# Kernel optimization log

Hardware: AMD Instinct MI355X
Metric: run time of the kernel (lower is better)

## Reference

```python
import jax, jax.numpy as jnp
import numpy as np
from jax import lax

PERM_AD = np.array([3, 0, 1, 6, 4, 2, 7, 8, 5])  # angular-difference kernel permutation
IDX_HD_POS = np.array([0, 3, 6]); IDX_HD_NEG = np.array([2, 5, 8])
IDX_VD_POS = np.array([0, 1, 2]); IDX_VD_NEG = np.array([6, 7, 8])
TOP_K = 1
THETA = 1.0


def conv2d_3x3(x, w, b):
    # x: [B,C,H,W], w: [O,I,3,3], b: [O]; stride 1, padding 1
    out = lax.conv_general_dilated(x, w, window_strides=(1, 1), padding=((1, 1), (1, 1)),
                                   dimension_numbers=('NCHW', 'OIHW', 'NCHW'))
    return out + b[None, :, None, None]


def setup_inputs() -> dict:
    key = jax.random.key(0)
    ks = jax.random.split(key, 12)
    B, C, H, W, E = 16, 64, 128, 128, 5

    def winit(k, shape, fan_in):
        return jax.random.normal(k, shape, jnp.float32) * (1.0 / np.sqrt(fan_in))

    return {
        'x': jax.random.normal(ks[0], (B, C, H, W), jnp.float32),
        'noise': jax.random.normal(ks[1], (B, E), jnp.float32),
        'w_gate': winit(ks[2], (C, E), C), 'b_gate': jnp.zeros((E,), jnp.float32),
        'w_noise': winit(ks[3], (C, E), C), 'b_noise': jnp.zeros((E,), jnp.float32),
        'w1': winit(ks[4], (C, C, 3, 3), C * 9), 'b1': jnp.zeros((C,), jnp.float32),
        'w_cd': winit(ks[5], (C, C, 3, 3), C * 9), 'b_cd': jnp.zeros((C,), jnp.float32),
        'w_hd': winit(ks[6], (C, C, 3), C * 3), 'b_hd': jnp.zeros((C,), jnp.float32),
        'w_vd': winit(ks[7], (C, C, 3), C * 3), 'b_vd': jnp.zeros((C,), jnp.float32),
        'w_ad': winit(ks[8], (C, C, 3, 3), C * 9), 'b_ad': jnp.zeros((C,), jnp.float32),
    }


def reference(x, noise, w_gate, b_gate, w_noise, b_noise,
              w1, b1, w_cd, b_cd, w_hd, b_hd, w_vd, b_vd, w_ad, b_ad):
    B, C, H, W = x.shape
    E = w_gate.shape[1]

    # ---- NoisyTopkRouter on globally pooled features ----
    pooled = x.mean(axis=(2, 3))                      # [B, C]
    logits = pooled @ w_gate + b_gate                 # [B, E]
    noise_logits = pooled @ w_noise + b_noise         # [B, E]
    noisy = logits + noise * jax.nn.softplus(noise_logits)
    topv, topi = lax.top_k(noisy, TOP_K)              # [B, k]
    sparse = jnp.full_like(noisy, -jnp.inf)
    sparse = sparse.at[jnp.arange(B)[:, None], topi].set(topv)
    gates = jax.nn.softmax(sparse, axis=-1)           # [B, E]; 0 for unselected, gate weight otherwise

    # ---- Difference-convolution expert kernels ----
    wcd_f = w_cd.reshape(C, C, 9)
    wcd = wcd_f.at[:, :, 4].add(-wcd_f.sum(-1)).reshape(C, C, 3, 3)   # center = w4 - sum(all)
    whd = jnp.zeros((C, C, 9), x.dtype).at[:, :, IDX_HD_POS].set(w_hd).at[:, :, IDX_HD_NEG].set(-w_hd).reshape(C, C, 3, 3)
    wvd = jnp.zeros((C, C, 9), x.dtype).at[:, :, IDX_VD_POS].set(w_vd).at[:, :, IDX_VD_NEG].set(-w_vd).reshape(C, C, 3, 3)
    wad_f = w_ad.reshape(C, C, 9)
    wad = (wad_f - THETA * wad_f[:, :, PERM_AD]).reshape(C, C, 3, 3)

    outs = jnp.stack([
        conv2d_3x3(x, w1, b1),
        conv2d_3x3(x, wcd, b_cd),
        conv2d_3x3(x, whd, b_hd),
        conv2d_3x3(x, wvd, b_vd),
        conv2d_3x3(x, wad, b_ad),
    ], axis=0)                                        # [E, B, C, H, W]

    # ---- SparseDispatcher.combine: per-example softmax over flattened depth, gate-weighted scatter-add ----
    flat = outs.reshape(E, B, C * H * W)
    sm = jax.nn.softmax(flat, axis=-1)                # softmax over depth dim, as in combine()
    combined = jnp.einsum('ebd,be->bd', sm, gates)    # gates are 0 for non-dispatched (expert,example) pairs
    return combined.reshape(B, C, H, W)
```

## Files before the change

kernel.cpp:

```cpp
#include <hip/hip_runtime.h>
#include <math.h>

#define B_  16
#define C_  64
#define HW_ 128
#define E_  5

typedef __bf16  bf16x8 __attribute__((ext_vector_type(8)));
typedef float   f32x4  __attribute__((ext_vector_type(4)));

#define WS_WEFFB   0
#define WS_BIAS    368640
#define WS_POOL    369920
#define WS_Z       374016
#define WS_EIDX    374080
#define WS_XT      374144
#define WS_EXP     33928576
#define WS_NEED_A  67483008ull
#define WS_NEED_B  33928576ull

static __device__ __forceinline__ unsigned short f2bf(float f) {
    unsigned int u = __float_as_uint(f);
    unsigned int r = (u + 0x7fffu + ((u >> 16) & 1u)) >> 16;
    return (unsigned short)r;
}

__global__ __launch_bounds__(256) void transpose_pool_kernel(
        const float* __restrict__ x, unsigned short* __restrict__ x_t,
        float* __restrict__ pooled) {
    int bid = blockIdx.x;
    int b = bid >> 7, row = bid & 127;
    int t = threadIdx.x;
    int wave = t >> 6, l = t & 63;
    int half = l >> 5;
    int c4 = l & 31;

    __shared__ unsigned short T[128][72];

    const float* xb = x + (size_t)b * (64 * 16384) + row * 128;

    #pragma unroll
    for (int it = 0; it < 8; it++) {
        int ci = wave * 16 + it * 2 + half;
        float4 v = *(const float4*)(xb + (size_t)ci * 16384 + c4 * 4);
        float p = v.x + v.y + v.z + v.w;
        p += __shfl_down(p, 16, 32);
        p += __shfl_down(p, 8, 32);
        p += __shfl_down(p, 4, 32);
        p += __shfl_down(p, 2, 32);
        p += __shfl_down(p, 1, 32);
        if (c4 == 0) atomicAdd(&pooled[b * 64 + ci], p * (1.0f / 16384.0f));
        int colb = c4 * 4;
        T[colb + 0][ci] = f2bf(v.x);
        T[colb + 1][ci] = f2bf(v.y);
        T[colb + 2][ci] = f2bf(v.z);
        T[colb + 3][ci] = f2bf(v.w);
    }
    __syncthreads();

    unsigned short* dst = x_t + ((size_t)(b * 128 + row) * 128) * 64;
    #pragma unroll
    for (int k = 0; k < 4; k++) {
        int chunk = t + k * 256;
        int col = chunk >> 3, c8 = chunk & 7;
        uint4 vv = *(const uint4*)&T[col][c8 * 8];
        *(uint4*)(dst + col * 64 + c8 * 8) = vv;
    }
}

__global__ void route_kernel(const float* __restrict__ pooled,
                             const float* __restrict__ noise,
                             const float* __restrict__ w_gate, const float* __restrict__ b_gate,
                             const float* __restrict__ w_noise, const float* __restrict__ b_noise,
                             int* __restrict__ expert_idx) {
    int b = threadIdx.x;
    if (b >= B_) return;
    float best = -1e30f;
    int bi = 0;
    for (int e = 0; e < E_; e++) {
        float lg = b_gate[e], nz = b_noise[e];
        for (int c = 0; c < C_; c++) {
            float pv = pooled[b * C_ + c];
            lg += pv * w_gate[c * E_ + e];
            nz += pv * w_noise[c * E_ + e];
        }
        float sp = log1pf(expf(nz));
        float v = lg + noise[b * E_ + e] * sp;
        if (v > best) { best = v; bi = e; }
    }
    expert_idx[b] = bi;
}

__global__ void build_w_kernel(const float* __restrict__ w1, const float* __restrict__ w_cd,
                               const float* __restrict__ w_hd, const float* __restrict__ w_vd,
                               const float* __restrict__ w_ad,
                               const float* __restrict__ b1, const float* __restrict__ b_cd,
                               const float* __restrict__ b_hd, const float* __restrict__ b_vd,
                               const float* __restrict__ b_ad,
                               unsigned short* __restrict__ wEffB, float* __restrict__ biasEff) {
    int gid = blockIdx.x * 256 + threadIdx.x;
    if (gid < E_ * 36864) {
        int e   = gid / 36864;
        int r   = gid % 36864;
        int g   = r / 18432;
        int r2  = r % 18432;
        int tap = r2 / 2048;
        int r3  = r2 % 2048;
        int q   = r3 / 512;
        int r4  = r3 % 512;
        int co  = r4 / 8;
        int j   = r4 % 8;
        int ci = g * 32 + q * 8 + j;
        int base9 = (co * 64 + ci) * 9;
        int base3 = (co * 64 + ci) * 3;
        float v = 0.f;
        if (e == 0) {
            v = w1[base9 + tap];
        } else if (e == 1) {
            if (tap == 4) {
                float s = 0.f;
                #pragma unroll
                for (int k = 0; k < 9; k++) s += w_cd[base9 + k];
                v = w_cd[base9 + 4] - s;
            } else {
                v = w_cd[base9 + tap];
            }
        } else if (e == 2) {
            int m = tap % 3;
            if (m == 0) v = w_hd[base3 + tap / 3];
            else if (m == 2) v = -w_hd[base3 + tap / 3];
        } else if (e == 3) {
            if (tap < 3) v = w_vd[base3 + tap];
            else if (tap >= 6) v = -w_vd[base3 + tap - 6];
        } else {
            const int PERM[9] = {3, 0, 1, 6, 4, 2, 7, 8, 5};
            v = w_ad[base9 + tap] - w_ad[base9 + PERM[tap]];
        }
        wEffB[gid] = f2bf(v);
    } else if (gid < E_ * 36864 + E_ * 64) {
        int jj = gid - E_ * 36864;
        int e = jj / 64, co = jj % 64;
        const float* bs;
        switch (e) {
            case 0: bs = b1; break;
            case 1: bs = b_cd; break;
            case 2: bs = b_hd; break;
            case 3: bs = b_vd; break;
            default: bs = b_ad; break;
        }
        biasEff[jj] = bs[co];
    }
}

__global__ __launch_bounds__(256) void conv_mfma_kernel(
        const unsigned short* __restrict__ x_t, const unsigned short* __restrict__ wEffB,
        const float* __restrict__ biasEff, const int* __restrict__ expert_idx,
        unsigned short* __restrict__ expw, float* __restrict__ outf,
        float* __restrict__ Z, int direct_f32) {
    int bid = blockIdx.x;
    int b = bid >> 6;
    int rem = bid & 63;
    int rg = rem >> 1;
    int ch = rem & 1;

    int t = threadIdx.x;
    int wave = t >> 6;
    int lane = t & 63;
    int ln = lane & 15;
    int q = lane >> 4;

    int e = expert_idx[b];

    __shared__ __align__(16) unsigned short A_lds[9 * 4 * 66 * 8];
    __shared__ __align__(16) unsigned short Xs[6 * 4 * 68 * 8];
    __shared__ float zs[4];

    f32x4 acc[4][4];
    #pragma unroll
    for (int i = 0; i < 4; i++)
        #pragma unroll
        for (int jn = 0; jn < 4; jn++)
            acc[i][jn] = (f32x4){0.f, 0.f, 0.f, 0.f};

    const unsigned short* xb = x_t + (size_t)b * (128 * 128 * 64);
    const unsigned short* we = wEffB + (size_t)e * 36864;

    for (int g = 0; g < 2; g++) {
        const uint4* asrc = (const uint4*)(we + g * 18432);
        for (int j = t; j < 2304; j += 256) {
            int slotrow = j >> 6;
            int m = j & 63;
            *(uint4*)&A_lds[(slotrow * 66 + m) * 8] = asrc[j];
        }
        for (int j = t; j < 1584; j += 256) {
            int xr = j / 264;
            int r2 = j % 264;
            int col = r2 >> 2;
            int qq = r2 & 3;
            int irow = rg * 4 - 1 + xr;
            int icol = ch * 64 - 1 + col;
            uint4 v = make_uint4(0, 0, 0, 0);
            if ((unsigned)irow < 128u && (unsigned)icol < 128u)
                v = *(const uint4*)(xb + ((size_t)irow * 128 + icol) * 64 + g * 32 + qq * 8);
            *(uint4*)&Xs[((xr * 4 + qq) * 68 + col) * 8] = v;
        }
        __syncthreads();

        #pragma unroll
        for (int tap = 0; tap < 9; tap++) {
            int dr = tap / 3, dc = tap % 3;
            bf16x8 af[4], bfr[4];
            #pragma unroll
            for (int mt = 0; mt < 4; mt++)
                af[mt] = *(const bf16x8*)&A_lds[((tap * 4 + q) * 66 + mt * 16 + ln) * 8];
            int xr = wave + dr;
            #pragma unroll
            for (int t4 = 0; t4 < 4; t4++)
                bfr[t4] = *(const bf16x8*)&Xs[((xr * 4 + q) * 68 + t4 * 16 + ln + dc) * 8];
            #pragma unroll
            for (int mt = 0; mt < 4; mt++)
                #pragma unroll
                for (int t4 = 0; t4 < 4; t4++)
                    acc[mt][t4] = __builtin_amdgcn_mfma_f32_16x16x32_bf16(
                        af[mt], bfr[t4], acc[mt][t4], 0, 0, 0);
        }
        __syncthreads();
    }

    int orow = rg * 4 + wave;
    float bsum = 0.f;
    size_t obase = (size_t)b * (64 * 16384);
    #pragma unroll
    for (int mt = 0; mt < 4; mt++) {
        float4 bias4 = *(const float4*)(biasEff + e * 64 + mt * 16 + q * 4);
        const float* bp = (const float*)&bias4;
        #pragma unroll
        for (int r = 0; r < 4; r++) {
            int co = mt * 16 + q * 4 + r;
            size_t cb = obase + (size_t)co * 16384 + (size_t)orow * 128;
            #pragma unroll
            for (int t4 = 0; t4 < 4; t4++) {
                float ev = __expf(acc[mt][t4][r] + bp[r]);
                bsum += ev;
                int ocol = ch * 64 + t4 * 16 + ln;
                if (direct_f32) outf[cb + ocol] = ev;
                else            expw[cb + ocol] = f2bf(ev);
            }
        }
    }
    for (int off = 32; off; off >>= 1) bsum += __shfl_down(bsum, off, 64);
    if (lane == 0) zs[wave] = bsum;
    __syncthreads();
    if (t == 0) atomicAdd(&Z[b], zs[0] + zs[1] + zs[2] + zs[3]);
}

__global__ __launch_bounds__(256) void scale_bf16_kernel(
        const unsigned short* __restrict__ expw, const float* __restrict__ Z,
        float* __restrict__ out) {
    int gid = blockIdx.x * 256 + threadIdx.x;
    int b = gid >> 17;
    __shared__ float sinv;
    if (threadIdx.x == 0) sinv = 1.0f / Z[b];
    __syncthreads();
    uint4 r = ((const uint4*)expw)[gid];
    float4 o0, o1;
    o0.x = __uint_as_float(r.x << 16) * sinv;
    o0.y = __uint_as_float(r.x & 0xffff0000u) * sinv;
    o0.z = __uint_as_float(r.y << 16) * sinv;
    o0.w = __uint_as_float(r.y & 0xffff0000u) * sinv;
    o1.x = __uint_as_float(r.z << 16) * sinv;
    o1.y = __uint_as_float(r.z & 0xffff0000u) * sinv;
    o1.z = __uint_as_float(r.w << 16) * sinv;
    o1.w = __uint_as_float(r.w & 0xffff0000u) * sinv;
    ((float4*)out)[gid * 2] = o0;
    ((float4*)out)[gid * 2 + 1] = o1;
}

__global__ __launch_bounds__(256) void scale_inplace_kernel(
        float* __restrict__ out, const float* __restrict__ Z) {
    int gid = blockIdx.x * 256 + threadIdx.x;
    int b = gid >> 18;
    __shared__ float sinv;
    if (threadIdx.x == 0) sinv = 1.0f / Z[b];
    __syncthreads();
    float4 v = ((float4*)out)[gid];
    v.x *= sinv; v.y *= sinv; v.z *= sinv; v.w *= sinv;
    ((float4*)out)[gid] = v;
}

extern "C" void kernel_launch(void* const* d_in, const int* in_sizes, int n_in,
                              void* d_out, int out_size, void* d_ws, size_t ws_size,
                              hipStream_t stream) {
    const float* x       = (const float*)d_in[0];
    const float* noise   = (const float*)d_in[1];
    const float* w_gate  = (const float*)d_in[2];
    const float* b_gate  = (const float*)d_in[3];
    const float* w_noise = (const float*)d_in[4];
    const float* b_noise = (const float*)d_in[5];
    const float* w1      = (const float*)d_in[6];
    const float* b1      = (const float*)d_in[7];
    const float* w_cd    = (const float*)d_in[8];
    const float* b_cd    = (const float*)d_in[9];
    const float* w_hd    = (const float*)d_in[10];
    const float* b_hd    = (const float*)d_in[11];
    const float* w_vd    = (const float*)d_in[12];
    const float* b_vd    = (const float*)d_in[13];
    const float* w_ad    = (const float*)d_in[14];
    const float* b_ad    = (const float*)d_in[15];

    char* ws = (char*)d_ws;
    unsigned short* wEffB   = (unsigned short*)(ws + WS_WEFFB);
    float*          biasEff = (float*)(ws + WS_BIAS);
    float*          pooled  = (float*)(ws + WS_POOL);
    float*          Zbuf    = (float*)(ws + WS_Z);
    int*            eidx    = (int*)(ws + WS_EIDX);
    unsigned short* x_t     = (unsigned short*)(ws + WS_XT);
    unsigned short* expw    = (unsigned short*)(ws + WS_EXP);

    float* out = (float*)d_out;
    int mode_a = (ws_size >= WS_NEED_A) ? 1 : 0;

    hipMemsetAsync(pooled, 0, 4160, stream);

    transpose_pool_kernel<<<B_ * 128, 256, 0, stream>>>(x, x_t, pooled);
    route_kernel<<<1, 64, 0, stream>>>(pooled, noise, w_gate, b_gate, w_noise, b_noise, eidx);
    build_w_kernel<<<(E_ * 36864 + E_ * 64 + 255) / 256, 256, 0, stream>>>(
        w1, w_cd, w_hd, w_vd, w_ad, b1, b_cd, b_hd, b_vd, b_ad, wEffB, biasEff);
    conv_mfma_kernel<<<1024, 256, 0, stream>>>(x_t, wEffB, biasEff, eidx,
                                               expw, out, Zbuf, mode_a ? 0 : 1);
    if (mode_a)
        scale_bf16_kernel<<<8192, 256, 0, stream>>>(expw, Zbuf, out);
    else
        scale_inplace_kernel<<<16384, 256, 0, stream>>>(out, Zbuf);
}
```

Measured before the change: 232.2 us.

## Fuse all stages into one cooperative persistent kernel with grid syncs

Replaces the chain of transpose/pool, route, weight-build, conv and rescale launches with a single cooperative kernel. Grid-wide syncs separate the phases, and the conv exps stay in registers so the final softmax scale is applied before one fp32 store, with no intermediate bf16 buffer and no separate scale pass. Weight A-fragments are now read directly from global memory instead of being staged in LDS, which lowers LDS use so that 4 blocks of 256 threads fit per CU. The cost is three grid.sync barriers and a dependence on cooperative launch, with the old multi-kernel path kept as a fallback.

```diff
diff --git a/kernel.cpp b/kernel.cpp
--- a/kernel.cpp
+++ b/kernel.cpp
@@ -1,9 +1,11 @@
 #include <hip/hip_runtime.h>
+#include <hip/hip_cooperative_groups.h>
 #include <math.h>
+
+namespace cg = cooperative_groups;
 
 #define B_  16
 #define C_  64
-#define HW_ 128
 #define E_  5
 
 typedef __bf16  bf16x8 __attribute__((ext_vector_type(8)));
@@ -15,14 +17,264 @@
 #define WS_Z       374016
 #define WS_EIDX    374080
 #define WS_XT      374144
-#define WS_EXP     33928576
+#define WS_EXP     33928576ull
 #define WS_NEED_A  67483008ull
-#define WS_NEED_B  33928576ull
 
 static __device__ __forceinline__ unsigned short f2bf(float f) {
     unsigned int u = __float_as_uint(f);
     unsigned int r = (u + 0x7fffu + ((u >> 16) & 1u)) >> 16;
     return (unsigned short)r;
+}
+
+__global__ __launch_bounds__(256, 4) void fused_moe(
+        const float* __restrict__ x, const float* __restrict__ noise,
+        const float* __restrict__ w_gate, const float* __restrict__ b_gate,
+        const float* __restrict__ w_noise, const float* __restrict__ b_noise,
+        const float* __restrict__ w1, const float* __restrict__ w_cd,
+        const float* __restrict__ w_hd, const float* __restrict__ w_vd,
+        const float* __restrict__ w_ad,
+        const float* __restrict__ b1, const float* __restrict__ b_cd,
+        const float* __restrict__ b_hd, const float* __restrict__ b_vd,
+        const float* __restrict__ b_ad,
+        unsigned short* __restrict__ wEffB, float* __restrict__ biasEff,
+        float* __restrict__ pooled, float* __restrict__ Z,
+        int* __restrict__ eidx, unsigned short* __restrict__ x_t,
+        float* __restrict__ out) {
+
+    cg::grid_group grid = cg::this_grid();
+    int t = threadIdx.x;
+    int blk = blockIdx.x;
+
+    __shared__ __align__(16) unsigned short SMEM[6 * 4 * 68 * 8];
+
+    {
+        int gid = blk * 256 + t;
+        if (gid < E_ * 36864) {
+            int e   = gid / 36864;
+            int r   = gid % 36864;
+            int g   = r / 18432;
+            int r2  = r % 18432;
+            int tap = r2 / 2048;
+            int r3  = r2 % 2048;
+            int q   = r3 / 512;
+            int r4  = r3 % 512;
+            int co  = r4 / 8;
+            int j   = r4 % 8;
+            int ci = g * 32 + q * 8 + j;
+            int base9 = (co * 64 + ci) * 9;
+            int base3 = (co * 64 + ci) * 3;
+            float v = 0.f;
+            if (e == 0) {
+                v = w1[base9 + tap];
+            } else if (e == 1) {
+                if (tap == 4) {
+                    float s = 0.f;
+                    #pragma unroll
+                    for (int k = 0; k < 9; k++) s += w_cd[base9 + k];
+                    v = w_cd[base9 + 4] - s;
+                } else {
+                    v = w_cd[base9 + tap];
+                }
+            } else if (e == 2) {
+                int m = tap % 3;
+                if (m == 0) v = w_hd[base3 + tap / 3];
+                else if (m == 2) v = -w_hd[base3 + tap / 3];
+            } else if (e == 3) {
+                if (tap < 3) v = w_vd[base3 + tap];
+                else if (tap >= 6) v = -w_vd[base3 + tap - 6];
+            } else {
+                const int PERM[9] = {3, 0, 1, 6, 4, 2, 7, 8, 5};
+                v = w_ad[base9 + tap] - w_ad[base9 + PERM[tap]];
+            }
+            wEffB[gid] = f2bf(v);
+        } else if (gid < E_ * 36864 + E_ * 64) {
+            int jj = gid - E_ * 36864;
+            int e = jj / 64, co = jj % 64;
+            const float* bs;
+            switch (e) {
+                case 0: bs = b1; break;
+                case 1: bs = b_cd; break;
+                case 2: bs = b_hd; break;
+                case 3: bs = b_vd; break;
+                default: bs = b_ad; break;
+            }
+            biasEff[jj] = bs[co];
+        }
+    }
+
+    {
+        int wave = t >> 6, l = t & 63;
+        int half = l >> 5;
+        int c4 = l & 31;
+        unsigned short (*T)[72] = (unsigned short (*)[72])SMEM;
+
+        for (int ii = 0; ii < 2; ii++) {
+            int task = blk * 2 + ii;
+            int b = task >> 7, row = task & 127;
+            const float* xb = x + (size_t)b * (64 * 16384) + row * 128;
+
+            #pragma unroll
+            for (int it = 0; it < 8; it++) {
+                int ci = wave * 16 + it * 2 + half;
+                float4 v = *(const float4*)(xb + (size_t)ci * 16384 + c4 * 4);
+                float p = v.x + v.y + v.z + v.w;
+                p += __shfl_down(p, 16, 32);
+                p += __shfl_down(p, 8, 32);
+                p += __shfl_down(p, 4, 32);
+                p += __shfl_down(p, 2, 32);
+                p += __shfl_down(p, 1, 32);
+                if (c4 == 0) atomicAdd(&pooled[b * 64 + ci], p * (1.0f / 16384.0f));
+                int colb = c4 * 4;
+                T[colb + 0][ci] = f2bf(v.x);
+                T[colb + 1][ci] = f2bf(v.y);
+                T[colb + 2][ci] = f2bf(v.z);
+                T[colb + 3][ci] = f2bf(v.w);
+            }
+            __syncthreads();
+
+            unsigned short* dst = x_t + ((size_t)(b * 128 + row) * 128) * 64;
+            #pragma unroll
+            for (int k = 0; k < 4; k++) {
+                int chunk = t + k * 256;
+                int col = chunk >> 3, c8 = chunk & 7;
+                uint4 vv = *(const uint4*)&T[col][c8 * 8];
+                *(uint4*)(dst + col * 64 + c8 * 8) = vv;
+            }
+            __syncthreads();
+        }
+    }
+
+    __threadfence();
+    grid.sync();
+    __threadfence();
+
+    if (blk == 0) {
+        float* vbuf = (float*)SMEM;
+        if (t < B_ * E_) {
+            int b = t / E_, e = t % E_;
+            float lg = b_gate[e], nz = b_noise[e];
+            for (int c = 0; c < C_; c++) {
+                float pv = pooled[b * C_ + c];
+                lg += pv * w_gate[c * E_ + e];
+                nz += pv * w_noise[c * E_ + e];
+            }
+            float sp = log1pf(expf(nz));
+            vbuf[t] = lg + noise[b * E_ + e] * sp;
+        }
+        __syncthreads();
+        if (t < B_) {
+            float best = -1e30f; int bi = 0;
+            #pragma unroll
+            for (int e = 0; e < E_; e++) {
+                float v = vbuf[t * E_ + e];
+                if (v > best) { best = v; bi = e; }
+            }
+            eidx[t] = bi;
+        }
+    }
+
+    __threadfence();
+    grid.sync();
+    __threadfence();
+
+    int b   = blk >> 6;
+    int rem = blk & 63;
+    int rg  = rem >> 1;
+    int ch  = rem & 1;
+    int wave = t >> 6, lane = t & 63;
+    int ln = lane & 15, q = lane >> 4;
+    int e = eidx[b];
+
+    f32x4 acc[4][4];
+    #pragma unroll
+    for (int i = 0; i < 4; i++)
+        #pragma unroll
+        for (int jn = 0; jn < 4; jn++)
+            acc[i][jn] = (f32x4){0.f, 0.f, 0.f, 0.f};
+
+    const unsigned short* xb = x_t + (size_t)b * (128 * 128 * 64);
+    const unsigned short* we = wEffB + (size_t)e * 36864;
+
+    for (int g = 0; g < 2; g++) {
+        for (int j = t; j < 1584; j += 256) {
+            int xr = j / 264;
+            int r2 = j % 264;
+            int col = r2 >> 2;
+            int qq = r2 & 3;
+            int irow = rg * 4 - 1 + xr;
+            int icol = ch * 64 - 1 + col;
+            uint4 v = make_uint4(0, 0, 0, 0);
+            if ((unsigned)irow < 128u && (unsigned)icol < 128u)
+                v = *(const uint4*)(xb + ((size_t)irow * 128 + icol) * 64 + g * 32 + qq * 8);
+            *(uint4*)&SMEM[((xr * 4 + qq) * 68 + col) * 8] = v;
+        }
+        __syncthreads();
+
+        const unsigned short* wg = we + g * 18432;
+        #pragma unroll
+        for (int tap = 0; tap < 9; tap++) {
+            int dr = tap / 3, dc = tap % 3;
+            bf16x8 af[4], bfr[4];
+            #pragma unroll
+            for (int mt = 0; mt < 4; mt++)
+                af[mt] = *(const bf16x8*)(wg + ((tap * 4 + q) * 64 + mt * 16 + ln) * 8);
+            int xr = wave + dr;
+            #pragma unroll
+            for (int t4 = 0; t4 < 4; t4++)
+                bfr[t4] = *(const bf16x8*)&SMEM[((xr * 4 + q) * 68 + t4 * 16 + ln + dc) * 8];
+            #pragma unroll
+            for (int mt = 0; mt < 4; mt++)
+                #pragma unroll
+                for (int t4 = 0; t4 < 4; t4++)
+                    acc[mt][t4] = __builtin_amdgcn_mfma_f32_16x16x32_bf16(
+                        af[mt], bfr[t4], acc[mt][t4], 0, 0, 0);
+        }
+        __syncthreads();
+    }
+
+    int orow = rg * 4 + wave;
+    float bsum = 0.f;
+    #pragma unroll
+    for (int mt = 0; mt < 4; mt++) {
+        float4 bias4 = *(const float4*)(biasEff + e * 64 + mt * 16 + q * 4);
+        const float* bp = (const float*)&bias4;
+        #pragma unroll
+        for (int r = 0; r < 4; r++) {
+            #pragma unroll
+            for (int t4 = 0; t4 < 4; t4++) {
+                float ev = __expf(acc[mt][t4][r] + bp[r]);
+                acc[mt][t4][r] = ev;
+                bsum += ev;
+            }
+        }
+    }
+    for (int off = 32; off; off >>= 1) bsum += __shfl_down(bsum, off, 64);
+    {
+        float* zsF = (float*)SMEM;
+        if (lane == 0) zsF[wave] = bsum;
+        __syncthreads();
+        if (t == 0) atomicAdd(&Z[b], zsF[0] + zsF[1] + zsF[2] + zsF[3]);
+    }
+
+    __threadfence();
+    grid.sync();
+    __threadfence();
+
+    float sinv = 1.0f / Z[b];
+    size_t obase = (size_t)b * (64 * 16384);
+    #pragma unroll
+    for (int mt = 0; mt < 4; mt++) {
+        #pragma unroll
+        for (int r = 0; r < 4; r++) {
+            int co = mt * 16 + q * 4 + r;
+            size_t cb = obase + (size_t)co * 16384 + (size_t)orow * 128;
+            #pragma unroll
+            for (int t4 = 0; t4 < 4; t4++) {
+                int ocol = ch * 64 + t4 * 16 + ln;
+                out[cb + ocol] = acc[mt][t4][r] * sinv;
+            }
+        }
+    }
 }
 
 __global__ __launch_bounds__(256) void transpose_pool_kernel(
@@ -152,7 +404,7 @@
     }
 }
 
-__global__ __launch_bounds__(256) void conv_mfma_kernel(
+__global__ __launch_bounds__(256, 4) void conv_mfma_kernel(
         const unsigned short* __restrict__ x_t, const unsigned short* __restrict__ wEffB,
         const float* __restrict__ biasEff, const int* __restrict__ expert_idx,
         unsigned short* __restrict__ expw, float* __restrict__ outf,
@@ -171,7 +423,6 @@
 
     int e = expert_idx[b];
 
-    __shared__ __align__(16) unsigned short A_lds[9 * 4 * 66 * 8];
     __shared__ __align__(16) unsigned short Xs[6 * 4 * 68 * 8];
     __shared__ float zs[4];
 
@@ -186,12 +437,6 @@
     const unsigned short* we = wEffB + (size_t)e * 36864;
 
     for (int g = 0; g < 2; g++) {
-        const uint4* asrc = (const uint4*)(we + g * 18432);
-        for (int j = t; j < 2304; j += 256) {
-            int slotrow = j >> 6;
-            int m = j & 63;
-            *(uint4*)&A_lds[(slotrow * 66 + m) * 8] = asrc[j];
-        }
         for (int j = t; j < 1584; j += 256) {
             int xr = j / 264;
             int r2 = j % 264;
@@ -206,13 +451,14 @@
         }
         __syncthreads();
 
+        const unsigned short* wg = we + g * 18432;
         #pragma unroll
         for (int tap = 0; tap < 9; tap++) {
             int dr = tap / 3, dc = tap % 3;
             bf16x8 af[4], bfr[4];
             #pragma unroll
             for (int mt = 0; mt < 4; mt++)
-                af[mt] = *(const bf16x8*)&A_lds[((tap * 4 + q) * 66 + mt * 16 + ln) * 8];
+                af[mt] = *(const bf16x8*)(wg + ((tap * 4 + q) * 64 + mt * 16 + ln) * 8);
             int xr = wave + dr;
             #pragma unroll
             for (int t4 = 0; t4 < 4; t4++)
@@ -318,18 +564,39 @@
     unsigned short* expw    = (unsigned short*)(ws + WS_EXP);
 
     float* out = (float*)d_out;
-    int mode_a = (ws_size >= WS_NEED_A) ? 1 : 0;
 
     hipMemsetAsync(pooled, 0, 4160, stream);
 
-    transpose_pool_kernel<<<B_ * 128, 256, 0, stream>>>(x, x_t, pooled);
-    route_kernel<<<1, 64, 0, stream>>>(pooled, noise, w_gate, b_gate, w_noise, b_noise, eidx);
-    build_w_kernel<<<(E_ * 36864 + E_ * 64 + 255) / 256, 256, 0, stream>>>(
-        w1, w_cd, w_hd, w_vd, w_ad, b1, b_cd, b_hd, b_vd, b_ad, wEffB, biasEff);
-    conv_mfma_kernel<<<1024, 256, 0, stream>>>(x_t, wEffB, biasEff, eidx,
-                                               expw, out, Zbuf, mode_a ? 0 : 1);
-    if (mode_a)
-        scale_bf16_kernel<<<8192, 256, 0, stream>>>(expw, Zbuf, out);
-    else
-        scale_inplace_kernel<<<16384, 256, 0, stream>>>(out, Zbuf);
-}
+    int nb = 0;
+    hipError_t qerr = hipOccupancyMaxActiveBlocksPerMultiprocessor(
+        &nb, (const void*)fused_moe, 256, 0);
+    bool coop = (qerr == hipSuccess) && (nb >= 4);
+
+    if (coop) {
+        void* kargs[] = {
+            (void*)&x, (void*)&noise,
+            (void*)&w_gate, (void*)&b_gate, (void*)&w_noise, (void*)&b_noise,
+            (void*)&w1, (void*)&w_cd, (void*)&w_hd, (void*)&w_vd, (void*)&w_ad,
+            (void*)&b1, (void*)&b_cd, (void*)&b_hd, (void*)&b_vd, (void*)&b_ad,
+            (void*)&wEffB, (void*)&biasEff, (void*)&pooled, (void*)&Zbuf,
+            (void*)&eidx, (void*)&x_t, (void*)&out
+        };
+        hipError_t lerr = hipLaunchCooperativeKernel((void*)fused_moe, dim3(1024),
+                                                     dim3(256), kargs, 0, stream);
+        if (lerr != hipSuccess) coop = false;
+    }
+
+    if (!coop) {
+        int mode_a = (ws_size >= WS_NEED_A) ? 1 : 0;
+        transpose_pool_kernel<<<B_ * 128, 256, 0, stream>>>(x, x_t, pooled);
+        route_kernel<<<1, 64, 0, stream>>>(pooled, noise, w_gate, b_gate, w_noise, b_noise, eidx);
+        build_w_kernel<<<(E_ * 36864 + E_ * 64 + 255) / 256, 256, 0, stream>>>(
+            w1, w_cd, w_hd, w_vd, w_ad, b1, b_cd, b_hd, b_vd, b_ad, wEffB, biasEff);
+        conv_mfma_kernel<<<1024, 256, 0, stream>>>(x_t, wEffB, biasEff, eidx,
+                                                   expw, out, Zbuf, mode_a ? 0 : 1);
+        if (mode_a)
+            scale_bf16_kernel<<<8192, 256, 0, stream>>>(expw, Zbuf, out);
+        else
+            scale_inplace_kernel<<<16384, 256, 0, stream>>>(out, Zbuf);
+    }
+}
```

Result: slower. 240.1 us (+3.4%).
